# Kernel optimization log

Hardware: AMD Instinct MI355X
Metric: run time of the kernel (lower is better)

The kernel has to match this reference:

```python
import jax, jax.numpy as jnp
import numpy as np

B, N, D = 8, 128, 768  # batch, max_units, input_dim
F = 3 * D + 2 * N - 1  # cat(2D) + multi(D) + rel_pos(2N-1)


def setup_inputs() -> dict:
    key = jax.random.key(0)
    k1, k2, k3, k4 = jax.random.split(key, 4)
    input_tensor = jax.random.normal(k1, (B, N, D), dtype=jnp.float32)
    unit_mask = jax.random.randint(k2, (B, N), 0, 2).astype(jnp.int32)
    # Linear(F, 1): weight [F], bias [1], init uniform(-0.05, 0.05) as in torch code
    W = jax.random.uniform(k3, (F,), minval=-0.05, maxval=0.05, dtype=jnp.float32)
    b = jax.random.uniform(k4, (1,), minval=-0.05, maxval=0.05, dtype=jnp.float32)
    return {"input_tensor": input_tensor, "W": W, "b": b, "unit_mask": unit_mask}


def reference(input_tensor, W, b, unit_mask):
    # Pair row (i, j) = [h_i ; h_j ; h_i*h_j ; onehot(j - i + N - 1)]
    # score[b,i,j] = h_i.w1 + h_j.w2 + (h_i*wm).h_j + wr[j-i+N-1] + bias
    # This is mathematically identical to building the [B,N,N,F] pair matrix
    # and applying Linear(F,1), but fused / never materialized.
    d = input_tensor.shape[-1]
    n = input_tensor.shape[1]
    w1, w2, wm, wr = W[:d], W[d:2 * d], W[2 * d:3 * d], W[3 * d:]

    si = input_tensor @ w1                                   # [B, N]  (h_i block)
    sj = input_tensor @ w2                                   # [B, N]  (h_j block)
    sm = jnp.einsum('bid,bjd->bij', input_tensor * wm, input_tensor)  # multi block
    idx = jnp.arange(n)
    rel = wr[idx[None, :] - idx[:, None] + n - 1]            # [N, N] rel-pos block

    scores = si[:, :, None] + sj[:, None, :] + sm + rel[None, :, :] + b[0]

    m = unit_mask.astype(bool)
    pair_mask = m[:, :, None] & m[:, None, :]                # row i valid AND col j valid
    neg_inf = jnp.array(-jnp.inf, dtype=scores.dtype)
    return jnp.where(pair_mask, scores, neg_inf)
```

## Files before the change

### kernel.cpp

```cpp
#include <hip/hip_runtime.h>
#include <hip/hip_bf16.h>


#define D 768
#define N 128
#define NEG_BIG (-3.0e38f)

typedef __attribute__((ext_vector_type(8))) short bf16x8;
typedef __attribute__((ext_vector_type(4))) float f32x4;

static __device__ __forceinline__ short b16(float f) {
  union { __hip_bfloat16 h; short s; } u;
  u.h = __float2bfloat16(f);
  return u.s;
}

__global__ __launch_bounds__(64) void fused_k(const float* __restrict__ X,
                                              const float* __restrict__ W,
                                              const float* __restrict__ bptr,
                                              const int* __restrict__ mask,
                                              float* __restrict__ out) {
  __shared__ float sils[16];
  const int lane = threadIdx.x;
  const int nt = blockIdx.x;
  const int mt = blockIdx.y;
  const int b  = blockIdx.z;
  const int r  = lane & 15;
  const int g  = lane >> 4;

  const float* xa = X + (b * N + mt * 16 + r) * D + g * 8;
  const float* xb = X + (b * N + nt * 16 + r) * D + g * 8;
  const float* w1 = W + g * 8;
  const float* w2 = W + D + g * 8;
  const float* wm = W + 2 * D + g * 8;

  f32x4 acc = {0.f, 0.f, 0.f, 0.f};
  float sa = 0.f, sb = 0.f;

#pragma unroll 4
  for (int kk = 0; kk < D; kk += 32) {
    const float4 a0 = *reinterpret_cast<const float4*>(xa + kk);
    const float4 a1 = *reinterpret_cast<const float4*>(xa + kk + 4);
    const float4 b0v = *reinterpret_cast<const float4*>(xb + kk);
    const float4 b1v = *reinterpret_cast<const float4*>(xb + kk + 4);
    const float4 m0 = *reinterpret_cast<const float4*>(wm + kk);
    const float4 m1 = *reinterpret_cast<const float4*>(wm + kk + 4);
    const float4 u0 = *reinterpret_cast<const float4*>(w1 + kk);
    const float4 u1 = *reinterpret_cast<const float4*>(w1 + kk + 4);
    const float4 v0 = *reinterpret_cast<const float4*>(w2 + kk);
    const float4 v1 = *reinterpret_cast<const float4*>(w2 + kk + 4);

    sa = fmaf(a0.x, u0.x, sa); sa = fmaf(a0.y, u0.y, sa);
    sa = fmaf(a0.z, u0.z, sa); sa = fmaf(a0.w, u0.w, sa);
    sa = fmaf(a1.x, u1.x, sa); sa = fmaf(a1.y, u1.y, sa);
    sa = fmaf(a1.z, u1.z, sa); sa = fmaf(a1.w, u1.w, sa);
    sb = fmaf(b0v.x, v0.x, sb); sb = fmaf(b0v.y, v0.y, sb);
    sb = fmaf(b0v.z, v0.z, sb); sb = fmaf(b0v.w, v0.w, sb);
    sb = fmaf(b1v.x, v1.x, sb); sb = fmaf(b1v.y, v1.y, sb);
    sb = fmaf(b1v.z, v1.z, sb); sb = fmaf(b1v.w, v1.w, sb);

    bf16x8 af, bf;
    af[0] = b16(a0.x * m0.x); af[1] = b16(a0.y * m0.y);
    af[2] = b16(a0.z * m0.z); af[3] = b16(a0.w * m0.w);
    af[4] = b16(a1.x * m1.x); af[5] = b16(a1.y * m1.y);
    af[6] = b16(a1.z * m1.z); af[7] = b16(a1.w * m1.w);
    bf[0] = b16(b0v.x); bf[1] = b16(b0v.y);
    bf[2] = b16(b0v.z); bf[3] = b16(b0v.w);
    bf[4] = b16(b1v.x); bf[5] = b16(b1v.y);
    bf[6] = b16(b1v.z); bf[7] = b16(b1v.w);

    acc = __builtin_amdgcn_mfma_f32_16x16x32_bf16(af, bf, acc, 0, 0, 0);
  }

  sa += __shfl_xor(sa, 16, 64);
  sa += __shfl_xor(sa, 32, 64);
  sb += __shfl_xor(sb, 16, 64);
  sb += __shfl_xor(sb, 32, 64);
  if (g == 0) sils[r] = sa;
  __syncthreads();
  const float4 siq = *reinterpret_cast<const float4*>(&sils[g * 4]);

  const float b0s = bptr[0];
  const int   j   = nt * 16 + r;
  const int   mj  = mask[b * N + j];
  const float* wr = W + 3 * D;
#pragma unroll
  for (int q = 0; q < 4; ++q) {
    const int   i  = mt * 16 + g * 4 + q;
    const int   mi = mask[b * N + i];
    const float v  = acc[q] + (&siq.x)[q] + sb + wr[j - i + N - 1] + b0s;
    out[(b * N + i) * N + j] = (mi && mj) ? v : NEG_BIG;
  }
}

extern "C" void kernel_launch(void* const* d_in, const int* in_sizes, int n_in,
                              void* d_out, int out_size, void* d_ws, size_t ws_size,
                              hipStream_t stream) {
  const float* X    = (const float*)d_in[0];
  const float* W    = (const float*)d_in[1];
  const float* bptr = (const float*)d_in[2];
  const int*   mask = (const int*)d_in[3];
  float* out = (float*)d_out;

  fused_k<<<dim3(8, 8, 8), 64, 0, stream>>>(X, W, bptr, mask, out);
}
```

Measured before the change: 15.39 us.

## Split K dimension across four waves per block with LDS reduction

Each block now runs four wavefronts, each covering a quarter of the 768-long feature dimension, instead of one wave looping over all of it. Partial MFMA tiles and the row/column dot products are written to shared memory, summed, and then each of the 256 threads writes one output element. The goal is to shorten the serial K loop and raise the number of waves in flight for this small 512-block grid. The cost is an extra LDS round trip and a block-wide barrier.

```diff
diff --git a/kernel.cpp b/kernel.cpp
--- a/kernel.cpp
+++ b/kernel.cpp
@@ -15,40 +15,45 @@
   return u.s;
 }
 
-__global__ __launch_bounds__(64) void fused_k(const float* __restrict__ X,
-                                              const float* __restrict__ W,
-                                              const float* __restrict__ bptr,
-                                              const int* __restrict__ mask,
-                                              float* __restrict__ out) {
-  __shared__ float sils[16];
-  const int lane = threadIdx.x;
+__global__ __launch_bounds__(256) void fused_k(const float* __restrict__ X,
+                                               const float* __restrict__ W,
+                                               const float* __restrict__ bptr,
+                                               const int* __restrict__ mask,
+                                               float* __restrict__ out) {
+  __shared__ float Cp[4][16][17];
+  __shared__ float Sr[4][16];
+  __shared__ float Sc[4][16];
+  const int tid  = threadIdx.x;
+  const int lane = tid & 63;
+  const int w    = tid >> 6;
+  const int r    = lane & 15;
+  const int g    = lane >> 4;
   const int nt = blockIdx.x;
   const int mt = blockIdx.y;
   const int b  = blockIdx.z;
-  const int r  = lane & 15;
-  const int g  = lane >> 4;
+  const int kb = w * 192;
 
-  const float* xa = X + (b * N + mt * 16 + r) * D + g * 8;
-  const float* xb = X + (b * N + nt * 16 + r) * D + g * 8;
-  const float* w1 = W + g * 8;
-  const float* w2 = W + D + g * 8;
-  const float* wm = W + 2 * D + g * 8;
+  const float* xa = X + (b * N + mt * 16 + r) * D + kb + g * 8;
+  const float* xb = X + (b * N + nt * 16 + r) * D + kb + g * 8;
+  const float* w1 = W + kb + g * 8;
+  const float* w2 = W + D + kb + g * 8;
+  const float* wm = W + 2 * D + kb + g * 8;
 
   f32x4 acc = {0.f, 0.f, 0.f, 0.f};
   float sa = 0.f, sb = 0.f;
 
-#pragma unroll 4
-  for (int kk = 0; kk < D; kk += 32) {
-    const float4 a0 = *reinterpret_cast<const float4*>(xa + kk);
-    const float4 a1 = *reinterpret_cast<const float4*>(xa + kk + 4);
+#pragma unroll
+  for (int kk = 0; kk < 192; kk += 32) {
+    const float4 a0  = *reinterpret_cast<const float4*>(xa + kk);
+    const float4 a1  = *reinterpret_cast<const float4*>(xa + kk + 4);
     const float4 b0v = *reinterpret_cast<const float4*>(xb + kk);
     const float4 b1v = *reinterpret_cast<const float4*>(xb + kk + 4);
-    const float4 m0 = *reinterpret_cast<const float4*>(wm + kk);
-    const float4 m1 = *reinterpret_cast<const float4*>(wm + kk + 4);
-    const float4 u0 = *reinterpret_cast<const float4*>(w1 + kk);
-    const float4 u1 = *reinterpret_cast<const float4*>(w1 + kk + 4);
-    const float4 v0 = *reinterpret_cast<const float4*>(w2 + kk);
-    const float4 v1 = *reinterpret_cast<const float4*>(w2 + kk + 4);
+    const float4 m0  = *reinterpret_cast<const float4*>(wm + kk);
+    const float4 m1  = *reinterpret_cast<const float4*>(wm + kk + 4);
+    const float4 u0  = *reinterpret_cast<const float4*>(w1 + kk);
+    const float4 u1  = *reinterpret_cast<const float4*>(w1 + kk + 4);
+    const float4 v0  = *reinterpret_cast<const float4*>(w2 + kk);
+    const float4 v1  = *reinterpret_cast<const float4*>(w2 + kk + 4);
 
     sa = fmaf(a0.x, u0.x, sa); sa = fmaf(a0.y, u0.y, sa);
     sa = fmaf(a0.z, u0.z, sa); sa = fmaf(a0.w, u0.w, sa);
@@ -59,38 +64,42 @@
     sb = fmaf(b1v.x, v1.x, sb); sb = fmaf(b1v.y, v1.y, sb);
     sb = fmaf(b1v.z, v1.z, sb); sb = fmaf(b1v.w, v1.w, sb);
 
-    bf16x8 af, bf;
+    bf16x8 af, bfv;
     af[0] = b16(a0.x * m0.x); af[1] = b16(a0.y * m0.y);
     af[2] = b16(a0.z * m0.z); af[3] = b16(a0.w * m0.w);
     af[4] = b16(a1.x * m1.x); af[5] = b16(a1.y * m1.y);
     af[6] = b16(a1.z * m1.z); af[7] = b16(a1.w * m1.w);
-    bf[0] = b16(b0v.x); bf[1] = b16(b0v.y);
-    bf[2] = b16(b0v.z); bf[3] = b16(b0v.w);
-    bf[4] = b16(b1v.x); bf[5] = b16(b1v.y);
-    bf[6] = b16(b1v.z); bf[7] = b16(b1v.w);
+    bfv[0] = b16(b0v.x); bfv[1] = b16(b0v.y);
+    bfv[2] = b16(b0v.z); bfv[3] = b16(b0v.w);
+    bfv[4] = b16(b1v.x); bfv[5] = b16(b1v.y);
+    bfv[6] = b16(b1v.z); bfv[7] = b16(b1v.w);
 
-    acc = __builtin_amdgcn_mfma_f32_16x16x32_bf16(af, bf, acc, 0, 0, 0);
+    acc = __builtin_amdgcn_mfma_f32_16x16x32_bf16(af, bfv, acc, 0, 0, 0);
   }
 
   sa += __shfl_xor(sa, 16, 64);
   sa += __shfl_xor(sa, 32, 64);
   sb += __shfl_xor(sb, 16, 64);
   sb += __shfl_xor(sb, 32, 64);
-  if (g == 0) sils[r] = sa;
+  if (g == 0) { Sr[w][r] = sa; Sc[w][r] = sb; }
+
+#pragma unroll
+  for (int q = 0; q < 4; ++q) Cp[w][g * 4 + q][r] = acc[q];
   __syncthreads();
-  const float4 siq = *reinterpret_cast<const float4*>(&sils[g * 4]);
 
-  const float b0s = bptr[0];
-  const int   j   = nt * 16 + r;
-  const int   mj  = mask[b * N + j];
+  const int row = tid >> 4;
+  const int col = tid & 15;
+  const float c  = Cp[0][row][col] + Cp[1][row][col] +
+                   Cp[2][row][col] + Cp[3][row][col];
+  const float si = Sr[0][row] + Sr[1][row] + Sr[2][row] + Sr[3][row];
+  const float sj = Sc[0][col] + Sc[1][col] + Sc[2][col] + Sc[3][col];
+  const int i = mt * 16 + row;
+  const int j = nt * 16 + col;
+  const int mi = mask[b * N + i];
+  const int mj = mask[b * N + j];
   const float* wr = W + 3 * D;
-#pragma unroll
-  for (int q = 0; q < 4; ++q) {
-    const int   i  = mt * 16 + g * 4 + q;
-    const int   mi = mask[b * N + i];
-    const float v  = acc[q] + (&siq.x)[q] + sb + wr[j - i + N - 1] + b0s;
-    out[(b * N + i) * N + j] = (mi && mj) ? v : NEG_BIG;
-  }
+  const float v = c + si + sj + wr[j - i + N - 1] + bptr[0];
+  out[(b * N + i) * N + j] = (mi && mj) ? v : NEG_BIG;
 }
 
 extern "C" void kernel_launch(void* const* d_in, const int* in_sizes, int n_in,
@@ -102,5 +111,5 @@
   const int*   mask = (const int*)d_in[3];
   float* out = (float*)d_out;
 
-  fused_k<<<dim3(8, 8, 8), 64, 0, stream>>>(X, W, bptr, mask, out);
+  fused_k<<<dim3(8, 8, 8), 256, 0, stream>>>(X, W, bptr, mask, out);
 }
```

Measured after the change: 13.99 us. -9.1%, faster.
